# Kernel tuning notes

Hardware: AMD Instinct MI355X
Metric: run time of the kernel (lower is better)

The kernel has to match this reference:

```python
import jax, jax.numpy as jnp
import numpy as np

VOCAB, EMBED, HIDDEN, NUM_CLASSES, PAD_IDX = 50257, 128, 128, 4, 0
B, T = 256, 512


def setup_inputs() -> dict:
    key = jax.random.key(0)
    ks = jax.random.split(key, 10)
    x = jax.random.randint(ks[0], (B, T), 0, VOCAB)
    h0 = jnp.zeros((B, HIDDEN), dtype=jnp.float32)
    # embedding: uniform(-0.1, 0.1), pad row zeroed (matches init_weights)
    emb = jax.random.uniform(ks[1], (VOCAB, EMBED), jnp.float32, -0.1, 0.1)
    emb = emb.at[PAD_IDX].set(0.0)
    def xavier(k, shape):
        fan_out, fan_in = shape
        bound = float(np.sqrt(6.0 / (fan_in + fan_out)))
        return jax.random.uniform(k, shape, jnp.float32, -bound, bound)
    W_ih = xavier(ks[2], (HIDDEN, EMBED))      # rnn.weight_ih_l0
    W_hh = xavier(ks[3], (HIDDEN, HIDDEN))     # rnn.weight_hh_l0
    b_ih = jnp.zeros((HIDDEN,), jnp.float32)
    b_hh = jnp.zeros((HIDDEN,), jnp.float32)
    W1 = xavier(ks[4], (2 * HIDDEN, HIDDEN))   # output_layer1
    b1 = jnp.zeros((2 * HIDDEN,), jnp.float32)
    W2 = xavier(ks[5], (NUM_CLASSES, 2 * HIDDEN))  # output_layer2
    b2 = jnp.zeros((NUM_CLASSES,), jnp.float32)
    return {"x": x, "h0": h0, "emb": emb, "W_ih": W_ih, "W_hh": W_hh,
            "b_ih": b_ih, "b_hh": b_hh, "W1": W1, "b1": b1, "W2": W2, "b2": b2}


def reference(x, h0, emb, W_ih, W_hh, b_ih, b_hh, W1, b1, W2, b2):
    # Embedding lookup (dropout layers are identity in eval mode)
    embedded = emb[x]                                    # [B, T, E]
    # Precompute input projection for every step, then scan the recurrence.
    x_proj = jnp.einsum('bte,he->bth', embedded, W_ih) + b_ih + b_hh  # [B, T, H]
    x_proj_t = jnp.swapaxes(x_proj, 0, 1)                # [T, B, H]

    def step(h, xp):
        h_new = jnp.tanh(xp + h @ W_hh.T)                # [B, H]
        return h_new, None

    last_hidden, _ = jax.lax.scan(step, h0, x_proj_t)    # [B, H]
    # MLP head: Linear -> ReLU -> Linear
    hidden_mlp = jax.nn.relu(last_hidden @ W1.T + b1)    # [B, 2H]
    logits = hidden_mlp @ W2.T + b2                      # [B, C]
    return (logits, last_hidden)
```

## Files before the change

kernel.cpp:

```cpp
#include <hip/hip_runtime.h>
#include <hip/hip_bf16.h>
#include <math.h>

#define BB 256
#define TT 512
#define EE 128
#define HH 128
#define NC 4
#define MM (BB * TT)

typedef __bf16 bf16x8 __attribute__((ext_vector_type(8)));
typedef __bf16 bf16x4 __attribute__((ext_vector_type(4)));
typedef float  f32x4  __attribute__((ext_vector_type(4)));
typedef float  f32x2  __attribute__((ext_vector_type(2)));

__device__ __forceinline__ float fast_tanh(float x) {
    float t = __builtin_amdgcn_exp2f(x * 2.885390081777927f);
    return 1.f - 2.f * __builtin_amdgcn_rcpf(1.f + t);
}

__device__ __forceinline__ void lds_barrier() {
    asm volatile("s_waitcnt lgkmcnt(0)" ::: "memory");
    __builtin_amdgcn_s_barrier();
    asm volatile("" ::: "memory");
}

__device__ __forceinline__ float xor16_sum(float p) {
    float t1 = p, t2 = p;
    asm volatile("v_permlane16_swap_b32 %0, %1" : "+v"(t1), "+v"(t2));
    return t1 + t2;
}
__device__ __forceinline__ float xor32_sum(float p) {
    float t1 = p, t2 = p;
    asm volatile("v_permlane32_swap_b32 %0, %1" : "+v"(t1), "+v"(t2));
    return t1 + t2;
}

template <typename XPT>
__global__ __launch_bounds__(256, 2) void embed_gemm(
    const int* __restrict__ x, const float* __restrict__ emb,
    const float* __restrict__ Wih, const float* __restrict__ bih,
    const float* __restrict__ bhh, XPT* __restrict__ xpout)
{
    const int tid = threadIdx.x;
    const int m0  = blockIdx.x * 128;

    const int LDA = 72;
    __shared__ __bf16 Ah[128 * 72];
    __shared__ __bf16 Al[128 * 72];
    __shared__ __bf16 Wh[128 * 72];
    __shared__ __bf16 Wl[128 * 72];
    __shared__ float  bias_s[128];
    __shared__ int    gix[128];

    if (tid < 128) {
        gix[tid]    = x[m0 + tid];
        bias_s[tid] = bih[tid] + bhh[tid];
    }

    const int lane = tid & 63, wid = tid >> 6;
    const int col  = lane & 15, quad = lane >> 4;

    f32x4 acc[2][8];
#pragma unroll
    for (int mt = 0; mt < 2; ++mt)
#pragma unroll
        for (int nt = 0; nt < 8; ++nt) acc[mt][nt] = f32x4{0.f, 0.f, 0.f, 0.f};

    __syncthreads();

#pragma unroll
    for (int half = 0; half < 2; ++half) {
#pragma unroll
        for (int it = 0; it < 8; ++it) {
            int c   = it * 256 + tid;
            int row = c >> 4;
            int seg = c & 15;

            float4 wv = ((const float4*)Wih)[row * 32 + half * 16 + seg];
            bf16x4 wh, wl;
            wh[0] = (__bf16)wv.x; wl[0] = (__bf16)(wv.x - (float)wh[0]);
            wh[1] = (__bf16)wv.y; wl[1] = (__bf16)(wv.y - (float)wh[1]);
            wh[2] = (__bf16)wv.z; wl[2] = (__bf16)(wv.z - (float)wh[2]);
            wh[3] = (__bf16)wv.w; wl[3] = (__bf16)(wv.w - (float)wh[3]);
            *(bf16x4*)&Wh[row * LDA + seg * 4] = wh;
            *(bf16x4*)&Wl[row * LDA + seg * 4] = wl;

            int gi = gix[row];
            float4 av = ((const float4*)emb)[(size_t)gi * 32 + half * 16 + seg];
            bf16x4 ah, al;
            ah[0] = (__bf16)av.x; al[0] = (__bf16)(av.x - (float)ah[0]);
            ah[1] = (__bf16)av.y; al[1] = (__bf16)(av.y - (float)ah[1]);
            ah[2] = (__bf16)av.z; al[2] = (__bf16)(av.z - (float)ah[2]);
            ah[3] = (__bf16)av.w; al[3] = (__bf16)(av.w - (float)ah[3]);
            *(bf16x4*)&Ah[row * LDA + seg * 4] = ah;
            *(bf16x4*)&Al[row * LDA + seg * 4] = al;
        }
        __syncthreads();

#pragma unroll
        for (int kk = 0; kk < 2; ++kk) {
            bf16x8 afh[2], afl[2];
#pragma unroll
            for (int mt = 0; mt < 2; ++mt) {
                int ro = (wid * 32 + mt * 16 + col) * LDA + kk * 32 + quad * 8;
                afh[mt] = *(const bf16x8*)&Ah[ro];
                afl[mt] = *(const bf16x8*)&Al[ro];
            }
#pragma unroll
            for (int nt = 0; nt < 8; ++nt) {
                int ro = (nt * 16 + col) * LDA + kk * 32 + quad * 8;
                bf16x8 wfh = *(const bf16x8*)&Wh[ro];
                bf16x8 wfl = *(const bf16x8*)&Wl[ro];
#pragma unroll
                for (int mt = 0; mt < 2; ++mt) {
                    acc[mt][nt] = __builtin_amdgcn_mfma_f32_16x16x32_bf16(afh[mt], wfh, acc[mt][nt], 0, 0, 0);
                    acc[mt][nt] = __builtin_amdgcn_mfma_f32_16x16x32_bf16(afl[mt], wfh, acc[mt][nt], 0, 0, 0);
                    acc[mt][nt] = __builtin_amdgcn_mfma_f32_16x16x32_bf16(afh[mt], wfl, acc[mt][nt], 0, 0, 0);
                }
            }
        }
        if (half == 0) __syncthreads();
    }

#pragma unroll
    for (int mt = 0; mt < 2; ++mt) {
#pragma unroll
        for (int nt = 0; nt < 8; ++nt) {
            int m = m0 + wid * 32 + mt * 16 + quad * 4;
            int n = nt * 16 + col;
            float bs = bias_s[n];
#pragma unroll
            for (int r = 0; r < 4; ++r)
                xpout[(size_t)(m + r) * 128 + n] = (XPT)(acc[mt][nt][r] + bs);
        }
    }
}

template <typename XPT>
__global__ __launch_bounds__(256, 1) void rnn_scan(
    const XPT* __restrict__ xp, const float* __restrict__ Whh,
    const float* __restrict__ h0, float* __restrict__ hlast)
{
    const int b    = blockIdx.x;
    const int tid  = threadIdx.x;
    const int w    = tid >> 6;
    const int lane = tid & 63;
    const int oo   = lane & 15;
    const int kq   = lane >> 4;

    const int A = w * 32 + oo;
    const int Bo = A + 16;

    __shared__ float h_s[2][128];

    f32x4 wA[8], wB[8];
#pragma unroll
    for (int uu = 0; uu < 8; ++uu) {
        int ul = (uu + 8 - kq) & 7;
        wA[uu] = *(const f32x4*)(Whh + (size_t)A  * 128 + kq * 32 + ul * 4);
        wB[uu] = *(const f32x4*)(Whh + (size_t)Bo * 128 + kq * 32 + ul * 4);
    }
#pragma unroll
    for (int c = 0; c < 8; ++c)
        asm volatile("" : "+v"(wA[c]), "+v"(wB[c]));

    if (tid < 128) {
        int q = tid >> 5, u = (tid >> 2) & 7, e = tid & 3;
        h_s[0][q * 32 + ((u + q) & 7) * 4 + e] = h0[b * 128 + tid];
    }

    const int wiA = w * 32 + (((oo >> 2) + w) & 7) * 4 + (oo & 3);
    const int wiB = w * 32 + ((4 + (oo >> 2) + w) & 7) * 4 + (oo & 3);

    const XPT* xpb = xp + (size_t)b * (TT * 128);
    float xvA[8], xvB[8];
#pragma unroll
    for (int s = 0; s < 8; ++s) {
        xvA[s] = (float)xpb[s * 128 + A];
        xvB[s] = (float)xpb[s * 128 + Bo];
    }
    lds_barrier();

    for (int tw = 0; tw < TT; tw += 8) {
#pragma unroll
        for (int ts = 0; ts < 8; ++ts) {
            const int c = ts & 1;
            const float* hq = &h_s[c][kq * 32];
            f32x4 h4[8];
#pragma unroll
            for (int uu = 0; uu < 8; ++uu) h4[uu] = *(const f32x4*)&hq[uu * 4];

            f32x4 sA = f32x4{0.f, 0.f, 0.f, 0.f};
            f32x4 sB = f32x4{0.f, 0.f, 0.f, 0.f};
#pragma unroll
            for (int uu = 0; uu < 8; ++uu) {
                sA += wA[uu] * h4[uu];
                sB += wB[uu] * h4[uu];
            }
            float pA = (sA[0] + sA[1]) + (sA[2] + sA[3]);
            float pB = (sB[0] + sB[1]) + (sB[2] + sB[3]);
            pA = xor16_sum(pA);  pB = xor16_sum(pB);
            pA = xor32_sum(pA);  pB = xor32_sum(pB);

            float hA = fast_tanh(pA + xvA[ts]);
            float hB = fast_tanh(pB + xvB[ts]);
            if (kq == 0) {
                h_s[c ^ 1][wiA] = hA;
                h_s[c ^ 1][wiB] = hB;
            }
            if (tw + 8 < TT) {
                xvA[ts] = (float)xpb[(size_t)(tw + 8 + ts) * 128 + A];
                xvB[ts] = (float)xpb[(size_t)(tw + 8 + ts) * 128 + Bo];
            }
            lds_barrier();
        }
    }
    if (tid < 128) {
        int q = tid >> 5, u = (tid >> 2) & 7, e = tid & 3;
        hlast[b * 128 + tid] = h_s[0][q * 32 + ((u + q) & 7) * 4 + e];
    }
}

__global__ __launch_bounds__(256, 2) void mlp_head(
    const float* __restrict__ hlast, const float* __restrict__ W1,
    const float* __restrict__ b1, const float* __restrict__ W2,
    const float* __restrict__ b2, float* __restrict__ out)
{
    const int b = blockIdx.x, tid = threadIdx.x;
    __shared__ float h_row[128];
    __shared__ float hid[256];

    if (tid < 128) {
        float hv = hlast[b * 128 + tid];
        h_row[tid] = hv;
        out[1024 + b * 128 + tid] = hv;
    }
    __syncthreads();

    {
        float acc = b1[tid];
        const float4* wrow = (const float4*)(W1 + (size_t)tid * 128);
#pragma unroll
        for (int k4 = 0; k4 < 32; ++k4) {
            float4 wv = wrow[k4];
            acc += wv.x * h_row[k4 * 4 + 0] + wv.y * h_row[k4 * 4 + 1]
                 + wv.z * h_row[k4 * 4 + 2] + wv.w * h_row[k4 * 4 + 3];
        }
        hid[tid] = fmaxf(acc, 0.f);
    }
    __syncthreads();

    const int wv = tid >> 6, lane = tid & 63;
    float s = 0.f;
#pragma unroll
    for (int qq = 0; qq < 4; ++qq)
        s += hid[qq * 64 + lane] * W2[wv * 256 + qq * 64 + lane];
#pragma unroll
    for (int off = 32; off > 0; off >>= 1) s += __shfl_down(s, off);
    if (lane == 0) out[b * 4 + wv] = s + b2[wv];
}

extern "C" void kernel_launch(void* const* d_in, const int* in_sizes, int n_in,
                              void* d_out, int out_size, void* d_ws, size_t ws_size,
                              hipStream_t stream)
{
    const int*   x   = (const int*)d_in[0];
    const float* h0  = (const float*)d_in[1];
    const float* emb = (const float*)d_in[2];
    const float* Wih = (const float*)d_in[3];
    const float* Whh = (const float*)d_in[4];
    const float* bih = (const float*)d_in[5];
    const float* bhh = (const float*)d_in[6];
    const float* W1  = (const float*)d_in[7];
    const float* b1  = (const float*)d_in[8];
    const float* W2  = (const float*)d_in[9];
    const float* b2  = (const float*)d_in[10];
    float* out = (float*)d_out;

    const size_t xp_f32_bytes = (size_t)MM * 128 * sizeof(float);
    const size_t hl_bytes     = (size_t)BB * 128 * sizeof(float);

    if (ws_size >= xp_f32_bytes + hl_bytes) {
        float* xpw = (float*)d_ws;
        float* hl  = (float*)((char*)d_ws + xp_f32_bytes);
        embed_gemm<float><<<MM / 128, 256, 0, stream>>>(x, emb, Wih, bih, bhh, xpw);
        rnn_scan<float><<<BB, 256, 0, stream>>>(xpw, Whh, h0, hl);
        mlp_head<<<BB, 256, 0, stream>>>(hl, W1, b1, W2, b2, out);
    } else {
        __bf16* xpw = (__bf16*)d_ws;
        float*  hl  = (float*)((char*)d_ws + (size_t)MM * 128 * sizeof(__bf16));
        embed_gemm<__bf16><<<MM / 128, 256, 0, stream>>>(x, emb, Wih, bih, bhh, xpw);
        rnn_scan<__bf16><<<BB, 256, 0, stream>>>(xpw, Whh, h0, hl);
        mlp_head<<<BB, 256, 0, stream>>>(hl, W1, b1, W2, b2, out);
    }
}
```

Before: 279.3 us.

## Fuse embedding gather and input projection into the recurrent scan kernel

After: 363.6 us. +30.2%, slower.

```diff
diff --git a/kernel.cpp b/kernel.cpp
--- a/kernel.cpp
+++ b/kernel.cpp
@@ -7,12 +7,8 @@
 #define EE 128
 #define HH 128
 #define NC 4
-#define MM (BB * TT)
-
-typedef __bf16 bf16x8 __attribute__((ext_vector_type(8)));
-typedef __bf16 bf16x4 __attribute__((ext_vector_type(4)));
-typedef float  f32x4  __attribute__((ext_vector_type(4)));
-typedef float  f32x2  __attribute__((ext_vector_type(2)));
+
+typedef float f32x4 __attribute__((ext_vector_type(4)));
 
 __device__ __forceinline__ float fast_tanh(float x) {
     float t = __builtin_amdgcn_exp2f(x * 2.885390081777927f);
@@ -36,110 +32,10 @@
     return t1 + t2;
 }
 
-template <typename XPT>
-__global__ __launch_bounds__(256, 2) void embed_gemm(
+__global__ __launch_bounds__(256, 1) void rnn_scan_fused(
     const int* __restrict__ x, const float* __restrict__ emb,
-    const float* __restrict__ Wih, const float* __restrict__ bih,
-    const float* __restrict__ bhh, XPT* __restrict__ xpout)
-{
-    const int tid = threadIdx.x;
-    const int m0  = blockIdx.x * 128;
-
-    const int LDA = 72;
-    __shared__ __bf16 Ah[128 * 72];
-    __shared__ __bf16 Al[128 * 72];
-    __shared__ __bf16 Wh[128 * 72];
-    __shared__ __bf16 Wl[128 * 72];
-    __shared__ float  bias_s[128];
-    __shared__ int    gix[128];
-
-    if (tid < 128) {
-        gix[tid]    = x[m0 + tid];
-        bias_s[tid] = bih[tid] + bhh[tid];
-    }
-
-    const int lane = tid & 63, wid = tid >> 6;
-    const int col  = lane & 15, quad = lane >> 4;
-
-    f32x4 acc[2][8];
-#pragma unroll
-    for (int mt = 0; mt < 2; ++mt)
-#pragma unroll
-        for (int nt = 0; nt < 8; ++nt) acc[mt][nt] = f32x4{0.f, 0.f, 0.f, 0.f};
-
-    __syncthreads();
-
-#pragma unroll
-    for (int half = 0; half < 2; ++half) {
-#pragma unroll
-        for (int it = 0; it < 8; ++it) {
-            int c   = it * 256 + tid;
-            int row = c >> 4;
-            int seg = c & 15;
-
-            float4 wv = ((const float4*)Wih)[row * 32 + half * 16 + seg];
-            bf16x4 wh, wl;
-            wh[0] = (__bf16)wv.x; wl[0] = (__bf16)(wv.x - (float)wh[0]);
-            wh[1] = (__bf16)wv.y; wl[1] = (__bf16)(wv.y - (float)wh[1]);
-            wh[2] = (__bf16)wv.z; wl[2] = (__bf16)(wv.z - (float)wh[2]);
-            wh[3] = (__bf16)wv.w; wl[3] = (__bf16)(wv.w - (float)wh[3]);
-            *(bf16x4*)&Wh[row * LDA + seg * 4] = wh;
-            *(bf16x4*)&Wl[row * LDA + seg * 4] = wl;
-
-            int gi = gix[row];
-            float4 av = ((const float4*)emb)[(size_t)gi * 32 + half * 16 + seg];
-            bf16x4 ah, al;
-            ah[0] = (__bf16)av.x; al[0] = (__bf16)(av.x - (float)ah[0]);
-            ah[1] = (__bf16)av.y; al[1] = (__bf16)(av.y - (float)ah[1]);
-            ah[2] = (__bf16)av.z; al[2] = (__bf16)(av.z - (float)ah[2]);
-            ah[3] = (__bf16)av.w; al[3] = (__bf16)(av.w - (float)ah[3]);
-            *(bf16x4*)&Ah[row * LDA + seg * 4] = ah;
-            *(bf16x4*)&Al[row * LDA + seg * 4] = al;
-        }
-        __syncthreads();
-
-#pragma unroll
-        for (int kk = 0; kk < 2; ++kk) {
-            bf16x8 afh[2], afl[2];
-#pragma unroll
-            for (int mt = 0; mt < 2; ++mt) {
-                int ro = (wid * 32 + mt * 16 + col) * LDA + kk * 32 + quad * 8;
-                afh[mt] = *(const bf16x8*)&Ah[ro];
-                afl[mt] = *(const bf16x8*)&Al[ro];
-            }
-#pragma unroll
-            for (int nt = 0; nt < 8; ++nt) {
-                int ro = (nt * 16 + col) * LDA + kk * 32 + quad * 8;
-                bf16x8 wfh = *(const bf16x8*)&Wh[ro];
-                bf16x8 wfl = *(const bf16x8*)&Wl[ro];
-#pragma unroll
-                for (int mt = 0; mt < 2; ++mt) {
-                    acc[mt][nt] = __builtin_amdgcn_mfma_f32_16x16x32_bf16(afh[mt], wfh, acc[mt][nt], 0, 0, 0);
-                    acc[mt][nt] = __builtin_amdgcn_mfma_f32_16x16x32_bf16(afl[mt], wfh, acc[mt][nt], 0, 0, 0);
-                    acc[mt][nt] = __builtin_amdgcn_mfma_f32_16x16x32_bf16(afh[mt], wfl, acc[mt][nt], 0, 0, 0);
-                }
-            }
-        }
-        if (half == 0) __syncthreads();
-    }
-
-#pragma unroll
-    for (int mt = 0; mt < 2; ++mt) {
-#pragma unroll
-        for (int nt = 0; nt < 8; ++nt) {
-            int m = m0 + wid * 32 + mt * 16 + quad * 4;
-            int n = nt * 16 + col;
-            float bs = bias_s[n];
-#pragma unroll
-            for (int r = 0; r < 4; ++r)
-                xpout[(size_t)(m + r) * 128 + n] = (XPT)(acc[mt][nt][r] + bs);
-        }
-    }
-}
-
-template <typename XPT>
-__global__ __launch_bounds__(256, 1) void rnn_scan(
-    const XPT* __restrict__ xp, const float* __restrict__ Whh,
+    const float* __restrict__ Wih, const float* __restrict__ Whh,
+    const float* __restrict__ bih, const float* __restrict__ bhh,
     const float* __restrict__ h0, float* __restrict__ hlast)
 {
     const int b    = blockIdx.x;
@@ -149,7 +45,7 @@
     const int oo   = lane & 15;
     const int kq   = lane >> 4;
 
-    const int A = w * 32 + oo;
+    const int A  = w * 32 + oo;
     const int Bo = A + 16;
 
     __shared__ float h_s[2][128];
@@ -161,24 +57,49 @@
         wA[uu] = *(const f32x4*)(Whh + (size_t)A  * 128 + kq * 32 + ul * 4);
         wB[uu] = *(const f32x4*)(Whh + (size_t)Bo * 128 + kq * 32 + ul * 4);
     }
-#pragma unroll
-    for (int c = 0; c < 8; ++c)
+    f32x4 iA[8], iB[8];
+#pragma unroll
+    for (int u = 0; u < 8; ++u) {
+        iA[u] = *(const f32x4*)(Wih + (size_t)A  * 128 + kq * 32 + u * 4);
+        iB[u] = *(const f32x4*)(Wih + (size_t)Bo * 128 + kq * 32 + u * 4);
+    }
+#pragma unroll
+    for (int c = 0; c < 8; ++c) {
         asm volatile("" : "+v"(wA[c]), "+v"(wB[c]));
+        asm volatile("" : "+v"(iA[c]), "+v"(iB[c]));
+    }
+
+    const float bsA = bih[A]  + bhh[A];
+    const float bsB = bih[Bo] + bhh[Bo];
 
     if (tid < 128) {
         int q = tid >> 5, u = (tid >> 2) & 7, e = tid & 3;
         h_s[0][q * 32 + ((u + q) & 7) * 4 + e] = h0[b * 128 + tid];
     }
 
-    const int wiA = w * 32 + (((oo >> 2) + w) & 7) * 4 + (oo & 3);
-    const int wiB = w * 32 + ((4 + (oo >> 2) + w) & 7) * 4 + (oo & 3);
-
-    const XPT* xpb = xp + (size_t)b * (TT * 128);
-    float xvA[8], xvB[8];
-#pragma unroll
-    for (int s = 0; s < 8; ++s) {
-        xvA[s] = (float)xpb[s * 128 + A];
-        xvB[s] = (float)xpb[s * 128 + Bo];
+    const int wrA = w * 32 + (((oo >> 2) + w) & 7) * 4 + (oo & 3);
+    const int wrB = w * 32 + ((4 + (oo >> 2) + w) & 7) * 4 + (oo & 3);
+
+    const int* xb = x + b * TT;
+    int xi[8];
+#pragma unroll
+    for (int s = 0; s < 8; ++s) xi[s] = xb[s];
+
+    f32x4 EB[8];
+    float xppA[2], xppB[2];
+    {
+        const float* er = emb + (size_t)xi[0] * 128 + kq * 32;
+#pragma unroll
+        for (int u = 0; u < 8; ++u) EB[u] = *(const f32x4*)(er + u * 4);
+        f32x4 sA = f32x4{0.f, 0.f, 0.f, 0.f};
+        f32x4 sB = f32x4{0.f, 0.f, 0.f, 0.f};
+#pragma unroll
+        for (int u = 0; u < 8; ++u) { sA += iA[u] * EB[u]; sB += iB[u] * EB[u]; }
+        xppA[0] = (sA[0] + sA[1]) + (sA[2] + sA[3]);
+        xppB[0] = (sB[0] + sB[1]) + (sB[2] + sB[3]);
+        er = emb + (size_t)xi[1] * 128 + kq * 32;
+#pragma unroll
+        for (int u = 0; u < 8; ++u) EB[u] = *(const f32x4*)(er + u * 4);
     }
     lds_barrier();
 
@@ -198,21 +119,31 @@
                 sA += wA[uu] * h4[uu];
                 sB += wB[uu] * h4[uu];
             }
-            float pA = (sA[0] + sA[1]) + (sA[2] + sA[3]);
-            float pB = (sB[0] + sB[1]) + (sB[2] + sB[3]);
+            float pA = (sA[0] + sA[1]) + (sA[2] + sA[3]) + xppA[c];
+            float pB = (sB[0] + sB[1]) + (sB[2] + sB[3]) + xppB[c];
+
+            {
+                f32x4 cA = f32x4{0.f, 0.f, 0.f, 0.f};
+                f32x4 cB = f32x4{0.f, 0.f, 0.f, 0.f};
+#pragma unroll
+                for (int u = 0; u < 8; ++u) { cA += iA[u] * EB[u]; cB += iB[u] * EB[u]; }
+                xppA[c ^ 1] = (cA[0] + cA[1]) + (cA[2] + cA[3]);
+                xppB[c ^ 1] = (cB[0] + cB[1]) + (cB[2] + cB[3]);
+                const float* er = emb + (size_t)xi[(ts + 2) & 7] * 128 + kq * 32;
+#pragma unroll
+                for (int u = 0; u < 8; ++u) EB[u] = *(const f32x4*)(er + u * 4);
+            }
+
             pA = xor16_sum(pA);  pB = xor16_sum(pB);
             pA = xor32_sum(pA);  pB = xor32_sum(pB);
 
-            float hA = fast_tanh(pA + xvA[ts]);
-            float hB = fast_tanh(pB + xvB[ts]);
+            float hA = fast_tanh(pA + bsA);
+            float hB = fast_tanh(pB + bsB);
             if (kq == 0) {
-                h_s[c ^ 1][wiA] = hA;
-                h_s[c ^ 1][wiB] = hB;
+                h_s[c ^ 1][wrA] = hA;
+                h_s[c ^ 1][wrB] = hB;
             }
-            if (tw + 8 < TT) {
-                xvA[ts] = (float)xpb[(size_t)(tw + 8 + ts) * 128 + A];
-                xvB[ts] = (float)xpb[(size_t)(tw + 8 + ts) * 128 + Bo];
-            }
+            if (tw + 8 < TT) xi[ts] = xb[tw + 8 + ts];
             lds_barrier();
         }
     }
@@ -278,20 +209,8 @@
     const float* b2  = (const float*)d_in[10];
     float* out = (float*)d_out;
 
-    const size_t xp_f32_bytes = (size_t)MM * 128 * sizeof(float);
-    const size_t hl_bytes     = (size_t)BB * 128 * sizeof(float);
-
-    if (ws_size >= xp_f32_bytes + hl_bytes) {
-        float* xpw = (float*)d_ws;
-        float* hl  = (float*)((char*)d_ws + xp_f32_bytes);
-        embed_gemm<float><<<MM / 128, 256, 0, stream>>>(x, emb, Wih, bih, bhh, xpw);
-        rnn_scan<float><<<BB, 256, 0, stream>>>(xpw, Whh, h0, hl);
-        mlp_head<<<BB, 256, 0, stream>>>(hl, W1, b1, W2, b2, out);
-    } else {
-        __bf16* xpw = (__bf16*)d_ws;
-        float*  hl  = (float*)((char*)d_ws + (size_t)MM * 128 * sizeof(__bf16));
-        embed_gemm<__bf16><<<MM / 128, 256, 0, stream>>>(x, emb, Wih, bih, bhh, xpw);
-        rnn_scan<__bf16><<<BB, 256, 0, stream>>>(xpw, Whh, h0, hl);
-        mlp_head<<<BB, 256, 0, stream>>>(hl, W1, b1, W2, b2, out);
-    }
-}
+    float* hl = (float*)d_ws;
+
+    rnn_scan_fused<<<BB, 256, 0, stream>>>(x, emb, Wih, Whh, bih, bhh, h0, hl);
+    mlp_head<<<BB, 256, 0, stream>>>(hl, W1, b1, W2, b2, out);
+}
```
